# Optimization experiments

Hardware: AMD Instinct MI355X
Metric: run time of the kernel (lower is better)

The kernel has to match this reference:

```python
import jax, jax.numpy as jnp
import numpy as np
import math

D_MODEL = 1024
N_HEADS = 16
DH = D_MODEL // N_HEADS
THETA = 10000.0


def _rope_tables(S):
    # freqs: (dh/2,)
    inv_freq = 1.0 / (THETA ** (jnp.arange(0, DH, 2, dtype=jnp.float32) / DH))
    ang = jnp.arange(S, dtype=jnp.float32)[:, None] * inv_freq[None, :]  # (S, dh/2)
    cos = jnp.concatenate([jnp.cos(ang), jnp.cos(ang)], axis=-1)  # (S, dh)
    sin = jnp.concatenate([jnp.sin(ang), jnp.sin(ang)], axis=-1)
    return cos, sin


def _apply_rope(x, cos, sin):
    # x: (B, S, H, dh); rotate-half RoPE
    x1, x2 = jnp.split(x, 2, axis=-1)
    rot = jnp.concatenate([-x2, x1], axis=-1)
    c = cos[None, :, None, :]
    s = sin[None, :, None, :]
    return x * c + rot * s


def setup_inputs() -> dict:
    key = jax.random.key(0)
    k1, k2, k3 = jax.random.split(key, 3)
    x = jax.random.normal(k1, (4, 2048, D_MODEL), dtype=jnp.float32)
    qkv = 0.01 * jax.random.normal(k2, (3 * D_MODEL, D_MODEL), dtype=jnp.float32)
    wo = 0.01 * jax.random.normal(k3, (D_MODEL, D_MODEL), dtype=jnp.float32)
    return {"x": x, "qkv": qkv, "wo": wo}


def reference(x, qkv, wo):
    B, S, D = x.shape
    QKV = x @ qkv.T  # (B, S, 3D)
    Q, K, V = jnp.split(QKV, 3, axis=-1)
    q = Q.reshape(B, S, N_HEADS, DH)
    k = K.reshape(B, S, N_HEADS, DH)
    v = V.reshape(B, S, N_HEADS, DH)
    cos, sin = _rope_tables(S)
    q = _apply_rope(q, cos, sin)
    k = _apply_rope(k, cos, sin)
    # (B, H, S, dh)
    q = q.transpose(0, 2, 1, 3)
    k = k.transpose(0, 2, 1, 3)
    v = v.transpose(0, 2, 1, 3)
    scores = jnp.einsum("bhsd,bhtd->bhst", q, k) / math.sqrt(float(DH))
    mask = jnp.tril(jnp.ones((S, S), dtype=scores.dtype))
    scores = scores * mask
    # faithful to original: any exact-zero entry (masked or incidental) -> -inf
    scores = jnp.where(scores == 0.0, -jnp.inf, scores)
    attn = jax.nn.softmax(scores, axis=-1)
    out = jnp.einsum("bhst,bhtd->bhsd", attn, v)  # (B, H, S, dh)
    out = out.transpose(0, 2, 1, 3).reshape(B, S, D)
    return out @ wo.T
```

## Files before the change

### kernel.cpp

```cpp
#include <hip/hip_runtime.h>
#include <math.h>

typedef __bf16 bf16x8 __attribute__((ext_vector_type(8)));
typedef __bf16 bf16x4 __attribute__((ext_vector_type(4)));
typedef float  floatx4 __attribute__((ext_vector_type(4)));
typedef float  floatx2 __attribute__((ext_vector_type(2)));

#define AS1(p) ((__attribute__((address_space(1))) void*)(p))
#define AS3(p) ((__attribute__((address_space(3))) void*)(p))

#define MASKV (-1.0e30f)
#define SOFTMAX_SCALE_LOG2 0.1803368801111244f
#define ROPE_LOG2F 0.4152410118609203f

__global__ __launch_bounds__(256)
void cvt3_kernel(const float* __restrict__ x, const float* __restrict__ qkv,
                 const float* __restrict__ wo, __bf16* __restrict__ xb,
                 __bf16* __restrict__ qkvb, __bf16* __restrict__ wob,
                 float* __restrict__ rt)
{
    const int bi = blockIdx.x;
    if (bi >= 12288) {
        const int e0 = (bi - 12288) * 1024 + threadIdx.x * 4;
#pragma unroll
        for (int j = 0; j < 4; ++j) {
            const int e = e0 + j;
            const int s = e >> 5, d = e & 31;
            const float f = exp2f(-(float)d * ROPE_LOG2F);
            float sn, cs;
            sincosf((float)s * f, &sn, &cs);
            floatx2 t; t[0] = cs; t[1] = sn;
            *(floatx2*)(rt + e * 2) = t;
        }
        return;
    }
    const float* src;
    __bf16* dst;
    int base;
    if (bi < 8192)       { src = x;   dst = xb;   base = bi * 1024; }
    else if (bi < 11264) { src = qkv; dst = qkvb; base = (bi - 8192) * 1024; }
    else                 { src = wo;  dst = wob;  base = (bi - 11264) * 1024; }

    const int i = base + threadIdx.x * 4;
    const floatx4 v = *(const floatx4*)(src + i);
    bf16x4 o;
    o[0] = (__bf16)v[0]; o[1] = (__bf16)v[1];
    o[2] = (__bf16)v[2]; o[3] = (__bf16)v[3];
    *(bf16x4*)(dst + i) = o;
}

__global__ __launch_bounds__(256)
void gemm_rope_kernel(const __bf16* __restrict__ A, const __bf16* __restrict__ BT,
                      __bf16* __restrict__ Qr, __bf16* __restrict__ Kr,
                      __bf16* __restrict__ Vt, const float* __restrict__ rt)
{
    const int K = 1024;
    __shared__ __align__(16) __bf16 As[128 * 32];
    __shared__ __align__(16) __bf16 Bs[128 * 32];

    const int tid  = threadIdx.x;
    const int wave = tid >> 6;
    const int lane = tid & 63;
    const int quad = lane >> 4;
    const int l16  = lane & 15;

    const long m0 = (long)blockIdx.y * 128;
    const long n0 = (long)blockIdx.x * 128;
    const int  wm = (wave >> 1) * 64;
    const int  wn = (wave & 1) * 64;

    floatx4 acc[4][4] = {};

    for (int k0 = 0; k0 < K; k0 += 32) {
#pragma unroll
        for (int t = 0; t < 2; ++t) {
            const int c   = (t * 4 + wave) * 64 + lane;
            const int row = c >> 2;
            const int kc  = (c & 3) * 8;
            const __bf16* ga = A  + (m0 + row) * (long)K + k0 + kc;
            const __bf16* gb = BT + (n0 + row) * (long)K + k0 + kc;
            __builtin_amdgcn_global_load_lds(AS1(ga), AS3(As + (t * 4 + wave) * 512), 16, 0, 0);
            __builtin_amdgcn_global_load_lds(AS1(gb), AS3(Bs + (t * 4 + wave) * 512), 16, 0, 0);
        }
        asm volatile("s_waitcnt vmcnt(0)" ::: "memory");
        __syncthreads();

        bf16x8 af[4], bfq[4];
#pragma unroll
        for (int mt = 0; mt < 4; ++mt)
            af[mt] = *(const bf16x8*)(As + (wm + mt * 16 + l16) * 32 + quad * 8);
#pragma unroll
        for (int nt = 0; nt < 4; ++nt)
            bfq[nt] = *(const bf16x8*)(Bs + (wn + nt * 16 + l16) * 32 + quad * 8);

#pragma unroll
        for (int mt = 0; mt < 4; ++mt)
#pragma unroll
            for (int nt = 0; nt < 4; ++nt)
                acc[mt][nt] = __builtin_amdgcn_mfma_f32_16x16x32_bf16(
                    af[mt], bfq[nt], acc[mt][nt], 0, 0, 0);
        __syncthreads();
    }

    const int gn0    = (int)n0 + wn;
    const int region = gn0 >> 10;
    const int h      = (gn0 >> 6) & 15;

    if (region == 2) {
#pragma unroll
        for (int mt = 0; mt < 4; ++mt) {
            const long gm = m0 + wm + mt * 16 + quad * 4;
            const int  b  = (int)(gm >> 11), s = (int)(gm & 2047);
#pragma unroll
            for (int nt = 0; nt < 4; ++nt) {
                const int d = nt * 16 + l16;
                bf16x4 w;
#pragma unroll
                for (int r = 0; r < 4; ++r) w[r] = (__bf16)acc[mt][nt][r];
                *(bf16x4*)(Vt + ((size_t)(b * 16 + h) * 64 + d) * 2048 + s) = w;
            }
        }
    } else {
        __bf16* dst = region ? Kr : Qr;
#pragma unroll
        for (int nt = 0; nt < 2; ++nt) {
            const int d1 = nt * 16 + l16;
#pragma unroll
            for (int mt = 0; mt < 4; ++mt) {
                const long gm0 = m0 + wm + mt * 16 + quad * 4;
                const int  b   = (int)(gm0 >> 11), s0 = (int)(gm0 & 2047);
#pragma unroll
                for (int r = 0; r < 4; ++r) {
                    const floatx2 t = *(const floatx2*)(rt + ((s0 + r) * 32 + d1) * 2);
                    const float a1 = acc[mt][nt][r];
                    const float a2 = acc[mt][nt + 2][r];
                    __bf16* row = dst + ((size_t)((b * 16 + h) * 2048 + s0 + r)) * 64;
                    row[d1]      = (__bf16)(a1 * t[0] - a2 * t[1]);
                    row[d1 + 32] = (__bf16)(a2 * t[0] + a1 * t[1]);
                }
            }
        }
    }
}

__global__ __launch_bounds__(256)
void gemm_bt_kernel(const __bf16* __restrict__ A, const __bf16* __restrict__ BT,
                    float* __restrict__ C, int M, int N, int K)
{
    __shared__ __align__(16) __bf16 As[128 * 32];
    __shared__ __align__(16) __bf16 Bs[128 * 32];

    const int tid  = threadIdx.x;
    const int wave = tid >> 6;
    const int lane = tid & 63;
    const int quad = lane >> 4;
    const int l16  = lane & 15;

    const long m0 = (long)blockIdx.y * 128;
    const long n0 = (long)blockIdx.x * 128;
    const int  wm = (wave >> 1) * 64;
    const int  wn = (wave & 1) * 64;

    floatx4 acc[4][4] = {};

    for (int k0 = 0; k0 < K; k0 += 32) {
#pragma unroll
        for (int t = 0; t < 2; ++t) {
            const int c   = (t * 4 + wave) * 64 + lane;
            const int row = c >> 2;
            const int kc  = (c & 3) * 8;
            const __bf16* ga = A  + (m0 + row) * (long)K + k0 + kc;
            const __bf16* gb = BT + (n0 + row) * (long)K + k0 + kc;
            __builtin_amdgcn_global_load_lds(AS1(ga), AS3(As + (t * 4 + wave) * 512), 16, 0, 0);
            __builtin_amdgcn_global_load_lds(AS1(gb), AS3(Bs + (t * 4 + wave) * 512), 16, 0, 0);
        }
        asm volatile("s_waitcnt vmcnt(0)" ::: "memory");
        __syncthreads();

        bf16x8 af[4], bfq[4];
#pragma unroll
        for (int mt = 0; mt < 4; ++mt)
            af[mt] = *(const bf16x8*)(As + (wm + mt * 16 + l16) * 32 + quad * 8);
#pragma unroll
        for (int nt = 0; nt < 4; ++nt)
            bfq[nt] = *(const bf16x8*)(Bs + (wn + nt * 16 + l16) * 32 + quad * 8);

#pragma unroll
        for (int mt = 0; mt < 4; ++mt)
#pragma unroll
            for (int nt = 0; nt < 4; ++nt)
                acc[mt][nt] = __builtin_amdgcn_mfma_f32_16x16x32_bf16(
                    af[mt], bfq[nt], acc[mt][nt], 0, 0, 0);
        __syncthreads();
    }

#pragma unroll
    for (int mt = 0; mt < 4; ++mt)
#pragma unroll
        for (int nt = 0; nt < 4; ++nt) {
            const long row = m0 + wm + mt * 16 + quad * 4;
            const long col = n0 + wn + nt * 16 + l16;
#pragma unroll
            for (int r = 0; r < 4; ++r)
                C[(row + r) * (long)N + col] = acc[mt][nt][r];
        }
}

__global__ __launch_bounds__(256, 4)
void attn_kernel(const __bf16* __restrict__ Qr, const __bf16* __restrict__ Kr,
                 const __bf16* __restrict__ Vt, __bf16* __restrict__ ctx)
{
    __shared__ __align__(16) __bf16 Ks[64 * 64];
    __shared__ __align__(16) __bf16 Vs[64 * 64];
    __shared__ __align__(16) __bf16 plds[4][16 * 72];

    const int bh   = blockIdx.x;
    const int b    = bh >> 4, h = bh & 15;
    const int tid  = threadIdx.x;
    const int wave = tid >> 6;
    const int lane = tid & 63;
    const int quad = lane >> 4, l16 = lane & 15;
    const int sw   = l16 & 7;

    const __bf16* Qb = Qr + (size_t)bh * 2048 * 64;
    const __bf16* Kb = Kr + (size_t)bh * 2048 * 64;
    const __bf16* Vb = Vt + (size_t)bh * 64 * 2048;
    __bf16* Pw = &plds[wave][0];

    const int c0   = tid;
    const int row0 = c0 >> 3, jg0 = (c0 & 7) ^ (row0 & 7);
    const int c1   = 256 + tid;
    const int row1 = c1 >> 3, jg1 = (c1 & 7) ^ (row1 & 7);

    const int tiles[2] = { (int)blockIdx.y, 31 - (int)blockIdx.y };

    for (int pass = 0; pass < 2; ++pass) {
        const int q0b  = tiles[pass] * 64;
        const int q0   = q0b + wave * 16;
        const int qa   = q0 + l16;
        const int kend = q0b + 64;

        bf16x8 bq[2];
#pragma unroll
        for (int t = 0; t < 2; ++t)
            bq[t] = *(const bf16x8*)(Qb + (q0 + l16) * 64 + t * 32 + quad * 8);

        floatx4 o[4] = {};
        float lpart = 0.f;

        for (int kt = 0; kt < kend; kt += 64) {
            __builtin_amdgcn_global_load_lds(AS1(Kb + (size_t)(kt + row0) * 64 + jg0 * 8),
                                             AS3(Ks + wave * 512), 16, 0, 0);
            __builtin_amdgcn_global_load_lds(AS1(Vb + (size_t)row0 * 2048 + kt + jg0 * 8),
                                             AS3(Vs + wave * 512), 16, 0, 0);
            __builtin_amdgcn_global_load_lds(AS1(Kb + (size_t)(kt + row1) * 64 + jg1 * 8),
                                             AS3(Ks + (4 + wave) * 512), 16, 0, 0);
            __builtin_amdgcn_global_load_lds(AS1(Vb + (size_t)row1 * 2048 + kt + jg1 * 8),
                                             AS3(Vs + (4 + wave) * 512), 16, 0, 0);
            asm volatile("s_waitcnt vmcnt(0)" ::: "memory");
            __syncthreads();

            floatx4 s[4] = {};
#pragma unroll
            for (int st = 0; st < 4; ++st) {
                bf16x8 ka0 = *(const bf16x8*)(Ks + (st * 16 + l16) * 64 + ((0 + quad) ^ sw) * 8);
                bf16x8 ka1 = *(const bf16x8*)(Ks + (st * 16 + l16) * 64 + ((4 + quad) ^ sw) * 8);
                s[st] = __builtin_amdgcn_mfma_f32_16x16x32_bf16(ka0, bq[0], s[st], 0, 0, 0);
                s[st] = __builtin_amdgcn_mfma_f32_16x16x32_bf16(ka1, bq[1], s[st], 0, 0, 0);
            }

#pragma unroll
            for (int st = 0; st < 4; ++st) {
                bf16x4 w;
#pragma unroll
                for (int r = 0; r < 4; ++r) {
                    const int key = kt + st * 16 + quad * 4 + r;
                    const float v = (key > qa) ? MASKV : s[st][r] * SOFTMAX_SCALE_LOG2;
                    const float p = __builtin_amdgcn_exp2f(v);
                    lpart += p;
                    w[r] = (__bf16)p;
                }
                *(bf16x4*)(Pw + l16 * 72 + st * 16 + quad * 4) = w;
            }

            asm volatile("s_waitcnt lgkmcnt(0)" ::: "memory");
            bf16x8 ap0 = *(const bf16x8*)(Pw + l16 * 72 + quad * 8);
            bf16x8 ap1 = *(const bf16x8*)(Pw + l16 * 72 + 32 + quad * 8);

#pragma unroll
            for (int nt = 0; nt < 4; ++nt) {
                bf16x8 bv0 = *(const bf16x8*)(Vs + (nt * 16 + l16) * 64 + ((0 + quad) ^ sw) * 8);
                bf16x8 bv1 = *(const bf16x8*)(Vs + (nt * 16 + l16) * 64 + ((4 + quad) ^ sw) * 8);
                o[nt] = __builtin_amdgcn_mfma_f32_16x16x32_bf16(ap0, bv0, o[nt], 0, 0, 0);
                o[nt] = __builtin_amdgcn_mfma_f32_16x16x32_bf16(ap1, bv1, o[nt], 0, 0, 0);
            }

            __syncthreads();
        }

        float l = lpart;
        l += __shfl_xor(l, 16, 64);
        l += __shfl_xor(l, 32, 64);
        float lr[4];
#pragma unroll
        for (int r = 0; r < 4; ++r)
            lr[r] = __shfl(l, quad * 4 + r, 64);
#pragma unroll
        for (int nt = 0; nt < 4; ++nt)
#pragma unroll
            for (int r = 0; r < 4; ++r) {
                const int srow = q0 + quad * 4 + r;
                const float inv_l = 1.0f / fmaxf(lr[r], 1e-20f);
                ctx[((size_t)(b * 2048 + srow)) * 1024 + h * 64 + nt * 16 + l16] =
                    (__bf16)(o[nt][r] * inv_l);
            }
    }
}

extern "C" void kernel_launch(void* const* d_in, const int* in_sizes, int n_in,
                              void* d_out, int out_size, void* d_ws, size_t ws_size,
                              hipStream_t stream)
{
    const float* x   = (const float*)d_in[0];
    const float* qkv = (const float*)d_in[1];
    const float* wo  = (const float*)d_in[2];
    float* out = (float*)d_out;

    char* ws = (char*)d_ws;
    const size_t MB = 1024 * 1024;
    __bf16* xb   = (__bf16*)(ws);
    __bf16* qkvb = (__bf16*)(ws + 16 * MB);
    __bf16* wob  = (__bf16*)(ws + 22 * MB);
    __bf16* Qr   = (__bf16*)(ws + 24 * MB);
    __bf16* Kr   = (__bf16*)(ws + 40 * MB);
    __bf16* Vt   = (__bf16*)(ws + 56 * MB);
    __bf16* ctx  = (__bf16*)(ws + 72 * MB);
    float*  rt   = (float*) (ws + 88 * MB);

    cvt3_kernel<<<12352, 256, 0, stream>>>(x, qkv, wo, xb, qkvb, wob, rt);
    gemm_rope_kernel<<<dim3(24, 64), 256, 0, stream>>>(xb, qkvb, Qr, Kr, Vt, rt);
    attn_kernel<<<dim3(64, 16), 256, 0, stream>>>(Qr, Kr, Vt, ctx);
    gemm_bt_kernel<<<dim3(8, 64), 256, 0, stream>>>(ctx, wob, out, 8192, 1024, 1024);
}
```

Measured before the change: 259.2 us.

## Double-buffer K/V tiles in attention and give each block four query tiles

Adds a second LDS buffer for the K and V tiles so the next tile's global-to-LDS load is issued before computing on the current one, overlapping memory latency with MFMA work. The grid is halved in y and each block now processes four query tiles in balanced pairs, which keeps causal work even and cuts the block count. Launch bounds drop from 4 to 3 blocks per CU because of the larger LDS footprint, so occupancy falls and there is less parallelism across CUs.

```diff
diff --git a/kernel.cpp b/kernel.cpp
--- a/kernel.cpp
+++ b/kernel.cpp
@@ -206,12 +206,23 @@
         }
 }
 
-__global__ __launch_bounds__(256, 4)
+#define STAGE(kt, bf)                                                                              \
+    do {                                                                                           \
+        __builtin_amdgcn_global_load_lds(AS1(Kb + (size_t)((kt) + row0) * 64 + jg0 * 8),           \
+                                         AS3(KV[bf][0] + wave * 512), 16, 0, 0);                   \
+        __builtin_amdgcn_global_load_lds(AS1(Vb + (size_t)row0 * 2048 + (kt) + jg0 * 8),           \
+                                         AS3(KV[bf][1] + wave * 512), 16, 0, 0);                   \
+        __builtin_amdgcn_global_load_lds(AS1(Kb + (size_t)((kt) + row1) * 64 + jg1 * 8),           \
+                                         AS3(KV[bf][0] + (4 + wave) * 512), 16, 0, 0);             \
+        __builtin_amdgcn_global_load_lds(AS1(Vb + (size_t)row1 * 2048 + (kt) + jg1 * 8),           \
+                                         AS3(KV[bf][1] + (4 + wave) * 512), 16, 0, 0);             \
+    } while (0)
+
+__global__ __launch_bounds__(256, 3)
 void attn_kernel(const __bf16* __restrict__ Qr, const __bf16* __restrict__ Kr,
                  const __bf16* __restrict__ Vt, __bf16* __restrict__ ctx)
 {
-    __shared__ __align__(16) __bf16 Ks[64 * 64];
-    __shared__ __align__(16) __bf16 Vs[64 * 64];
+    __shared__ __align__(16) __bf16 KV[2][2][64 * 64];
     __shared__ __align__(16) __bf16 plds[4][16 * 72];
 
     const int bh   = blockIdx.x;
@@ -232,9 +243,10 @@
     const int c1   = 256 + tid;
     const int row1 = c1 >> 3, jg1 = (c1 & 7) ^ (row1 & 7);
 
-    const int tiles[2] = { (int)blockIdx.y, 31 - (int)blockIdx.y };
-
-    for (int pass = 0; pass < 2; ++pass) {
+    const int ty = (int)blockIdx.y;
+    const int tiles[4] = { ty, 31 - ty, 8 + ty, 23 - ty };
+
+    for (int pass = 0; pass < 4; ++pass) {
         const int q0b  = tiles[pass] * 64;
         const int q0   = q0b + wave * 16;
         const int qa   = q0 + l16;
@@ -248,17 +260,17 @@
         floatx4 o[4] = {};
         float lpart = 0.f;
 
+        STAGE(0, 0);
+        asm volatile("s_waitcnt vmcnt(0)" ::: "memory");
+        __syncthreads();
+
+        int cur = 0;
         for (int kt = 0; kt < kend; kt += 64) {
-            __builtin_amdgcn_global_load_lds(AS1(Kb + (size_t)(kt + row0) * 64 + jg0 * 8),
-                                             AS3(Ks + wave * 512), 16, 0, 0);
-            __builtin_amdgcn_global_load_lds(AS1(Vb + (size_t)row0 * 2048 + kt + jg0 * 8),
-                                             AS3(Vs + wave * 512), 16, 0, 0);
-            __builtin_amdgcn_global_load_lds(AS1(Kb + (size_t)(kt + row1) * 64 + jg1 * 8),
-                                             AS3(Ks + (4 + wave) * 512), 16, 0, 0);
-            __builtin_amdgcn_global_load_lds(AS1(Vb + (size_t)row1 * 2048 + kt + jg1 * 8),
-                                             AS3(Vs + (4 + wave) * 512), 16, 0, 0);
-            asm volatile("s_waitcnt vmcnt(0)" ::: "memory");
-            __syncthreads();
+            if (kt + 64 < kend)
+                STAGE(kt + 64, cur ^ 1);
+
+            const __bf16* Ks = KV[cur][0];
+            const __bf16* Vs = KV[cur][1];
 
             floatx4 s[4] = {};
 #pragma unroll
@@ -295,7 +307,9 @@
                 o[nt] = __builtin_amdgcn_mfma_f32_16x16x32_bf16(ap1, bv1, o[nt], 0, 0, 0);
             }
 
+            asm volatile("s_waitcnt vmcnt(0)" ::: "memory");
             __syncthreads();
+            cur ^= 1;
         }
 
         float l = lpart;
@@ -339,6 +353,6 @@
 
     cvt3_kernel<<<12352, 256, 0, stream>>>(x, qkv, wo, xb, qkvb, wob, rt);
     gemm_rope_kernel<<<dim3(24, 64), 256, 0, stream>>>(xb, qkvb, Qr, Kr, Vt, rt);
-    attn_kernel<<<dim3(64, 16), 256, 0, stream>>>(Qr, Kr, Vt, ctx);
+    attn_kernel<<<dim3(64, 8), 256, 0, stream>>>(Qr, Kr, Vt, ctx);
     gemm_bt_kernel<<<dim3(8, 64), 256, 0, stream>>>(ctx, wob, out, 8192, 1024, 1024);
 }
```

After: 274.2 us. 5.8% more time.
